# Kernel optimization log

Measured on AMD Instinct MI355X. Metric: run time of the kernel, lower is better.

The kernel has to match this reference:

```python
import jax, jax.numpy as jnp
import numpy as np

N_NODES = 50000
N_EDGES = 800000
LATENT = 64
K_STEPS = 2
GAMMA = 0.9


def _xavier(key, fan_in, fan_out):
    lim = float(np.sqrt(6.0 / (fan_in + fan_out)))
    return jax.random.uniform(key, (fan_in, fan_out), minval=-lim, maxval=lim, dtype=jnp.float32)


def setup_inputs() -> dict:
    key = jax.random.key(0)
    ks = iter(jax.random.split(key, 48))
    L = LATENT
    inp = {}
    inp["x"] = jax.random.normal(next(ks), (N_NODES, 1), dtype=jnp.float32)
    inp["sol"] = jax.random.normal(next(ks), (N_NODES, 1), dtype=jnp.float32)
    inp["y"] = jax.random.normal(next(ks), (N_NODES, 1), dtype=jnp.float32)
    inp["tags"] = jax.random.randint(next(ks), (N_NODES,), 0, 2, dtype=jnp.int32)
    inp["edge_index"] = jax.random.randint(next(ks), (2, N_EDGES), 0, N_NODES, dtype=jnp.int32)
    inp["edge_attr"] = jax.random.normal(next(ks), (N_EDGES, 3), dtype=jnp.float32)
    inp["a_ij"] = jax.random.normal(next(ks), (N_EDGES,), dtype=jnp.float32)
    inp["prb_data"] = jax.random.normal(next(ks), (N_NODES, 2), dtype=jnp.float32)
    # phi_to / phi_from message MLPs: (2L+3) -> L -> L
    for name in ("pt", "pf"):
        inp[name + "_W1"] = _xavier(next(ks), 2 * L + 3, L)
        inp[name + "_b1"] = jnp.zeros((L,), jnp.float32)
        inp[name + "_W2"] = _xavier(next(ks), L, L)
        inp[name + "_b2"] = jnp.zeros((L,), jnp.float32)
    # gating MLPs: (3L+2) -> L, single linear + activation
    for name in ("zk", "rk", "corr"):
        inp[name + "_W"] = _xavier(next(ks), 3 * L + 2, L)
        inp[name + "_b"] = jnp.zeros((L,), jnp.float32)
    # encoder: 1 -> L -> L ; decoder: L -> L -> 1
    inp["e_W1"] = _xavier(next(ks), 1, L); inp["e_b1"] = jnp.zeros((L,), jnp.float32)
    inp["e_W2"] = _xavier(next(ks), L, L); inp["e_b2"] = jnp.zeros((L,), jnp.float32)
    inp["d_W1"] = _xavier(next(ks), L, L); inp["d_b1"] = jnp.zeros((L,), jnp.float32)
    inp["d_W2"] = _xavier(next(ks), L, 1); inp["d_b2"] = jnp.zeros((1,), jnp.float32)
    return inp


def reference(x, sol, y, tags, edge_index, edge_attr, a_ij, prb_data,
              pt_W1, pt_b1, pt_W2, pt_b2, pf_W1, pf_b1, pf_W2, pf_b2,
              zk_W, zk_b, rk_W, rk_b, corr_W, corr_b,
              e_W1, e_b1, e_W2, e_b2, d_W1, d_b1, d_W2, d_b2):
    n = x.shape[0]
    row, col = edge_index[0], edge_index[1]
    # remove_self_loops: mask out edges with row == col instead of slicing
    loop_mask = (row != col).astype(x.dtype)[:, None]

    def mlp2(t, W1, b1, W2, b2):  # Linear -> ReLU -> Linear
        return jnp.maximum(t @ W1 + b1, 0.0) @ W2 + b2

    def phi(h, i_idx, j_idx, W1, b1, W2, b2):
        # message = MLP([x_i, x_j, edge_attr]); aggr='add' at node i
        tmp = jnp.concatenate([h[i_idx], h[j_idx], edge_attr], axis=1)
        msg = mlp2(tmp, W1, b1, W2, b2) * loop_mask
        return jax.ops.segment_sum(msg, i_idx, num_segments=n)

    enc_p = (e_W1, e_b1, e_W2, e_b2)
    dec_p = (d_W1, d_b1, d_W2, d_b2)

    def apply(u, p):
        return mlp2(u, *p)

    def residual_loss(u):
        Au = jax.ops.segment_sum(a_ij[:, None] * u[col], row, num_segments=n)
        return jnp.mean((Au - y) ** 2)

    mse = lambda a, b: jnp.mean((a - b) ** 2)
    sg = lambda p: tuple(jax.lax.stop_gradient(t) for t in p)
    dir_mask = (tags == 1)[:, None]

    H0 = apply(x, enc_p)
    H = H0
    U = x
    total = jnp.float32(0.0)
    for step in range(K_STEPS):
        # phi_to: flow source->target => i = col (target); phi_from: i = row (source)
        mess_to = phi(H, col, row, pt_W1, pt_b1, pt_W2, pt_b2)
        mess_from = phi(H, row, col, pf_W1, pf_b1, pf_W2, pf_b2)
        cat = jnp.concatenate([H, mess_to, mess_from, prb_data], axis=1)
        alpha = jax.nn.sigmoid(cat @ zk_W + zk_b)
        reset = jax.nn.sigmoid(cat @ rk_W + rk_b)
        corr = jnp.tanh(
            jnp.concatenate([reset * H, mess_to, mess_from, prb_data], axis=1) @ corr_W + corr_b)
        Hn = H + alpha * corr
        Hn = jnp.where(dir_mask, H0, Hn)  # Dirichlet nodes reset to H['0']
        U = apply(Hn, dec_p)
        res = residual_loss(U)
        enc_loss = mse(apply(apply(Hn, sg(dec_p)), enc_p), Hn)        # 'latent'
        autoenc_loss = mse(apply(apply(U, sg(enc_p)), dec_p), U)      # 'physics'
        total = total + res * GAMMA ** (K_STEPS - step - 1) + enc_loss + autoenc_loss
        H = Hn
    return (U, total)
```

## Files before the change

### kernel.cpp

```cpp
#include <hip/hip_runtime.h>

#define DEV __device__ __forceinline__

constexpr int N = 50000;
constexpr int E = 800000;
constexpr int NBUK = 196;

constexpr int HF_OFF  = 0;
constexpr int H0F_OFF = 64*N;
constexpr int MTF_OFF = 128*N;
constexpr int MFF_OFF = 160*N;
constexpr int PBT_OFF = MTF_OFF;
constexpr int PBF_OFF = MFF_OFF;
constexpr int R1_OFF  = 192*N;
constexpr int PAT_OFF = R1_OFF;
constexpr int PAF_OFF = R1_OFF + 64*N;
constexpr int AL_OFF  = R1_OFF;
constexpr int RH_OFF  = R1_OFF + 64*N;
constexpr int T1_OFF  = R1_OFF;
constexpr int EV_OFF  = R1_OFF + 64*N;
constexpr int CSTG_OFF = R1_OFF;
constexpr int RSTG_OFF = R1_OFF + 4*E;
constexpr int HB_OFF   = 352*N;
constexpr int UV_OFF   = 384*N;
constexpr int LOSS_OFF = UV_OFF + N;
constexpr int FLAG_OFF = LOSS_OFF + 7;
constexpr int WZR_OFF = LOSS_OFF + 8;
constexpr int GB_OFF  = WZR_OFF + 24832;
constexpr int CW_OFF  = GB_OFF + 128;
constexpr int CB_OFF  = CW_OFF + 12416;
constexpr int PT1_OFF = CB_OFF + 64;
constexpr int AT_OFF  = PT1_OFF + 8192;
constexpr int BT1_OFF = AT_OFF + 192;
constexpr int WT2_OFF = BT1_OFF + 64;
constexpr int BT2_OFF = WT2_OFF + 4096;
constexpr int PF1_OFF = BT2_OFF + 64;
constexpr int AF_OFF  = PF1_OFF + 8192;
constexpr int BF1_OFF = AF_OFF + 192;
constexpr int WF2_OFF = BF1_OFF + 64;
constexpr int BF2_OFF = WF2_OFF + 4096;
constexpr int DW1_OFF = BF2_OFF + 64;
constexpr int DW2_OFF = DW1_OFF + 4096;
constexpr int DB1_OFF = DW2_OFF + 64;
constexpr int DB2_OFF = DB1_OFF + 64;
constexpr int EW1_OFF = DB2_OFF + 4;
constexpr int EB1_OFF = EW1_OFF + 64;
constexpr int EW2_OFF = EB1_OFF + 64;
constexpr int EB2_OFF = EW2_OFF + 4096;
constexpr int PRB0_OFF = EB2_OFF + 64;
constexpr int PRB1_OFF = PRB0_OFF + N;
constexpr int NWZR_OFF = PRB1_OFF + N;
constexpr int NCW_OFF  = NWZR_OFF + 25088;
constexpr int CNT_OFF  = NCW_OFF + 12544;
constexpr int FEND     = CNT_OFF + 2*N;
constexpr int CREC_OFF = FEND;
constexpr int RREC_OFF = CREC_OFF + 2*E;
constexpr int LCP_OFF  = RREC_OFF + 4*E;
constexpr int FRP_OFF  = LCP_OFF + N + 1;
constexpr int LE_OFF   = FRP_OFF + N + 1;
constexpr int LCF_OFF  = LE_OFF + N;
constexpr int LRF_OFF  = LCF_OFF + N;
constexpr int SFF_OFF  = LRF_OFF + N;
constexpr int CDEG_OFF = SFF_OFF + N;
constexpr int RDEG_OFF = CDEG_OFF + N;
constexpr int SDEG_OFF = RDEG_OFF + N;
constexpr int BS_OFF   = SDEG_OFF + N;
constexpr int BO_OFF   = BS_OFF + 512;
constexpr int GFC_OFF  = BO_OFF + 512;
constexpr int GFR_OFF  = GFC_OFF + 196;

constexpr int PREP_TOTAL = 24832+128+12416+64+8192+192+64+4096+64+8192+192+64+4096+64+4096+64+64+1+64+64+4096+64+6;
constexpr int PREP2_TOTAL = 25088 + 12544;

DEV float b2f(unsigned short u){ return __uint_as_float(((unsigned)u) << 16); }
DEV unsigned short f2b(float f){
    unsigned u = __float_as_uint(f);
    return (unsigned short)((u + 0x7fffu + ((u >> 16) & 1u)) >> 16);
}
DEV float blo(unsigned u){ return __uint_as_float(u << 16); }
DEV float bhi(unsigned u){ return __uint_as_float(u & 0xffff0000u); }
DEV int bcasti(int v, int k){ return __builtin_amdgcn_readlane(v, k); }
DEV float wave_sum(float v){
    #pragma unroll
    for (int off = 32; off > 0; off >>= 1) v += __shfl_xor(v, off, 64);
    return v;
}
DEV float ldv(const void* p, int i, bool isbf){
    return isbf ? b2f(((const unsigned short*)p)[i]) : ((const float*)p)[i];
}
DEV unsigned short ld16(const void* p, int i, bool isbf){
    return isbf ? ((const unsigned short*)p)[i] : f2b(((const float*)p)[i]);
}
DEV float sigm(float x){ return 1.f / (1.f + __expf(-x)); }

struct WPtrs {
    const void *ptW1, *ptb1, *ptW2, *ptb2;
    const void *pfW1, *pfb1, *pfW2, *pfb2;
    const void *zkW, *zkb, *rkW, *rkb, *cW, *cb;
    const void *eW1, *eb1, *eW2, *eb2;
    const void *dW1, *db1, *dW2, *db2;
};

__global__ __launch_bounds__(256) void detect_kernel(const void* y, float* __restrict__ ws){
    __shared__ int bad;
    if (threadIdx.x == 0) bad = 0;
    __syncthreads();
    const unsigned short* yy = (const unsigned short*)y;
    int mybad = 0;
    for (int i = threadIdx.x; i < 4096; i += 256){
        float v = b2f(yy[i]);
        if (!(v > -1.0e6f && v < 1.0e6f)) mybad = 1;
    }
    if (mybad) bad = 1;
    __syncthreads();
    if (threadIdx.x == 0) ws[FLAG_OFF] = bad ? 0.0f : 1.0f;
}

__global__ __launch_bounds__(256) void prep_kernel(WPtrs P, float* __restrict__ ws){
    int j = blockIdx.x * 256 + threadIdx.x;
    if (j >= PREP_TOTAL) return;
    bool isbf = ws[FLAG_OFF] > 0.5f;
    if (j < 24832){
        int k = j >> 7, c = j & 127;
        ws[WZR_OFF+j] = (c < 64) ? ldv(P.zkW, k*64+c, isbf) : ldv(P.rkW, k*64+(c-64), isbf);
        return;
    } j -= 24832;
    if (j < 128){ ws[GB_OFF+j] = (j < 64) ? ldv(P.zkb, j, isbf) : ldv(P.rkb, j-64, isbf); return; } j -= 128;
    if (j < 12416){ ws[CW_OFF+j] = ldv(P.cW, j, isbf); return; } j -= 12416;
    if (j < 64){ ws[CB_OFF+j] = ldv(P.cb, j, isbf); return; } j -= 64;
    if (j < 8192){ ws[PT1_OFF+j] = ldv(P.ptW1, j, isbf); return; } j -= 8192;
    if (j < 192){ ws[AT_OFF+j] = ldv(P.ptW1, 128*64+j, isbf); return; } j -= 192;
    if (j < 64){ ws[BT1_OFF+j] = ldv(P.ptb1, j, isbf); return; } j -= 64;
    if (j < 4096){ ws[WT2_OFF+j] = ldv(P.ptW2, j, isbf); return; } j -= 4096;
    if (j < 64){ ws[BT2_OFF+j] = ldv(P.ptb2, j, isbf); return; } j -= 64;
    if (j < 8192){ ws[PF1_OFF+j] = ldv(P.pfW1, j, isbf); return; } j -= 8192;
    if (j < 192){ ws[AF_OFF+j] = ldv(P.pfW1, 128*64+j, isbf); return; } j -= 192;
    if (j < 64){ ws[BF1_OFF+j] = ldv(P.pfb1, j, isbf); return; } j -= 64;
    if (j < 4096){ ws[WF2_OFF+j] = ldv(P.pfW2, j, isbf); return; } j -= 4096;
    if (j < 64){ ws[BF2_OFF+j] = ldv(P.pfb2, j, isbf); return; } j -= 64;
    if (j < 4096){ ws[DW1_OFF+j] = ldv(P.dW1, j, isbf); return; } j -= 4096;
    if (j < 64){ ws[DW2_OFF+j] = ldv(P.dW2, j, isbf); return; } j -= 64;
    if (j < 64){ ws[DB1_OFF+j] = ldv(P.db1, j, isbf); return; } j -= 64;
    if (j < 1){ ws[DB2_OFF] = ldv(P.db2, 0, isbf); return; } j -= 1;
    if (j < 64){ ws[EW1_OFF+j] = ldv(P.eW1, j, isbf); return; } j -= 64;
    if (j < 64){ ws[EB1_OFF+j] = ldv(P.eb1, j, isbf); return; } j -= 64;
    if (j < 4096){ ws[EW2_OFF+j] = ldv(P.eW2, j, isbf); return; } j -= 4096;
    if (j < 64){ ws[EB2_OFF+j] = ldv(P.eb2, j, isbf); return; } j -= 64;
    ws[LOSS_OFF+j] = 0.f;
}

__global__ __launch_bounds__(256) void prep2_kernel(float* __restrict__ ws){
    int j = blockIdx.x * 256 + threadIdx.x;
    if (j >= PREP2_TOTAL) return;
    if (j < 25088){
        int r = j >> 7, c = j & 127;
        float v;
        if (r < 64) v = ws[WZR_OFF + r*128 + c];
        else if (r < 128){
            int h = r - 64; float s = 0.f;
            for (int m = 0; m < 64; m++)
                s = fmaf(ws[WT2_OFF + h*64 + m], ws[WZR_OFF + (64+m)*128 + c], s);
            v = s;
        } else if (r < 192){
            int h = r - 128; float s = 0.f;
            for (int m = 0; m < 64; m++)
                s = fmaf(ws[WF2_OFF + h*64 + m], ws[WZR_OFF + (128+m)*128 + c], s);
            v = s;
        } else if (r < 194) v = ws[WZR_OFF + r*128 + c];
        else if (r == 194){
            float s = 0.f;
            for (int m = 0; m < 64; m++)
                s = fmaf(ws[BT2_OFF + m], ws[WZR_OFF + (64+m)*128 + c], s);
            v = s;
        } else {
            float s = 0.f;
            for (int m = 0; m < 64; m++)
                s = fmaf(ws[BF2_OFF + m], ws[WZR_OFF + (128+m)*128 + c], s);
            v = s;
        }
        ws[NWZR_OFF + j] = v;
        return;
    }
    j -= 25088;
    {
        int r = j >> 6, c = j & 63;
        float v;
        if (r < 64) v = ws[CW_OFF + r*64 + c];
        else if (r < 128){
            int h = r - 64; float s = 0.f;
            for (int m = 0; m < 64; m++)
                s = fmaf(ws[WT2_OFF + h*64 + m], ws[CW_OFF + (64+m)*64 + c], s);
            v = s;
        } else if (r < 192){
            int h = r - 128; float s = 0.f;
            for (int m = 0; m < 64; m++)
                s = fmaf(ws[WF2_OFF + h*64 + m], ws[CW_OFF + (128+m)*64 + c], s);
            v = s;
        } else if (r < 194) v = ws[CW_OFF + r*64 + c];
        else if (r == 194){
            float s = 0.f;
            for (int m = 0; m < 64; m++)
                s = fmaf(ws[BT2_OFF + m], ws[CW_OFF + (64+m)*64 + c], s);
            v = s;
        } else {
            float s = 0.f;
            for (int m = 0; m < 64; m++)
                s = fmaf(ws[BF2_OFF + m], ws[CW_OFF + (128+m)*64 + c], s);
            v = s;
        }
        ws[NCW_OFF + j] = v;
    }
}

__global__ __launch_bounds__(256) void setup_node(const void* __restrict__ prb, float* __restrict__ ws){
    int i = blockIdx.x * 256 + threadIdx.x;
    if (i >= N) return;
    bool isbf = ws[FLAG_OFF] > 0.5f;
    ws[PRB0_OFF+i] = ldv(prb, 2*i,   isbf);
    ws[PRB1_OFF+i] = ldv(prb, 2*i+1, isbf);
    int* wsI = (int*)ws;
    wsI[CDEG_OFF+i] = 0; wsI[RDEG_OFF+i] = 0; wsI[SDEG_OFF+i] = 0;
}

__global__ __launch_bounds__(256) void hist_kernel(const int* __restrict__ ei, int* __restrict__ wsI){
    int e = blockIdx.x * 256 + threadIdx.x;
    if (e >= E) return;
    int r = ei[e], c = ei[E+e];
    atomicAdd(&wsI[RDEG_OFF + r], 1);
    atomicAdd(&wsI[CDEG_OFF + c], 1);
    if (r == c) atomicAdd(&wsI[SDEG_OFF + r], 1);
}
DEV int deg_at(const int* wsI, int y, int i){
    if (y == 0) return wsI[CDEG_OFF+i] - wsI[SDEG_OFF+i];
    return wsI[RDEG_OFF+i];
}
__global__ __launch_bounds__(256) void scan1(int* __restrict__ wsI){
    int y = blockIdx.y;
    int* tmp = wsI + (y == 0 ? LCP_OFF : FRP_OFF);
    int i = blockIdx.x * 256 + threadIdx.x;
    __shared__ int sh[256];
    int v = (i < N) ? deg_at(wsI, y, i) : 0;
    sh[threadIdx.x] = v;
    __syncthreads();
    #pragma unroll
    for (int off = 1; off < 256; off <<= 1){
        int t = (threadIdx.x >= (unsigned)off) ? sh[threadIdx.x - off] : 0;
        __syncthreads();
        sh[threadIdx.x] += t;
        __syncthreads();
    }
    if (i < N) tmp[i] = sh[threadIdx.x] - v;
    if (threadIdx.x == 255) wsI[BS_OFF + y*256 + blockIdx.x] = sh[255];
}
__global__ __launch_bounds__(256) void scan2(int* __restrict__ wsI){
    int y = blockIdx.y, t = threadIdx.x;
    __shared__ int sh[256];
    int v = (t < 196) ? wsI[BS_OFF + y*256 + t] : 0;
    sh[t] = v;
    __syncthreads();
    #pragma unroll
    for (int off = 1; off < 256; off <<= 1){
        int u = (t >= (unsigned)off) ? sh[t - off] : 0;
        __syncthreads();
        sh[t] += u;
        __syncthreads();
    }
    wsI[BO_OFF + y*256 + t] = sh[t] - v;
}
__global__ __launch_bounds__(256) void scan3(int* __restrict__ wsI){
    int y = blockIdx.y;
    int* ptr = wsI + (y == 0 ? LCP_OFF : FRP_OFF);
    int i = blockIdx.x * 256 + threadIdx.x;
    if (i < N){
        int d = deg_at(wsI, y, i);
        int p = ptr[i] + wsI[BO_OFF + y*256 + blockIdx.x];
        ptr[i] = p;
        if ((i & 255) == 0){
            if (y == 0) wsI[GFC_OFF + (i >> 8)] = p;
            else        wsI[GFR_OFF + (i >> 8)] = p;
        }
        if (y == 0){
            wsI[LCF_OFF+i] = p;
            if (i == N-1) ptr[N] = p + d;
        } else {
            int live = wsI[RDEG_OFF+i] - wsI[SDEG_OFF+i];
            wsI[LRF_OFF+i] = p;
            wsI[LE_OFF+i]  = p + live;
            wsI[SFF_OFF+i] = p + live;
            if (i == N-1) ptr[N] = E;
        }
    }
}

__global__ __launch_bounds__(256) void scatter_binA(const int* __restrict__ ei,
                                                    const void* __restrict__ attr,
                                                    const void* __restrict__ aij,
                                                    float* __restrict__ ws){
    __shared__ int hc[NBUK], hr[NBUK], bc[NBUK], br[NBUK];
    int t = threadIdx.x;
    for (int i = t; i < NBUK; i += 256){ hc[i] = 0; hr[i] = 0; }
    __syncthreads();
    int* wsI = (int*)ws;
    int e0 = blockIdx.x * 4096;
    for (int i = 0; i < 16; i++){
        int e = e0 + i*256 + t;
        if (e < E){
            int r = ei[e], c = ei[E+e];
            if (r != c) atomicAdd(&hc[c >> 8], 1);
            atomicAdd(&hr[r >> 8], 1);
        }
    }
    __syncthreads();
    if (t < NBUK){
        bc[t] = atomicAdd(&wsI[GFC_OFF+t], hc[t]);
        br[t] = atomicAdd(&wsI[GFR_OFF+t], hr[t]);
        hc[t] = 0; hr[t] = 0;
    }
    __syncthreads();
    bool isbf = ws[FLAG_OFF] > 0.5f;
    uint4* cstg = (uint4*)(ws + CSTG_OFF);
    uint4* rstg = (uint4*)(ws + RSTG_OFF);
    for (int i = 0; i < 16; i++){
        int e = e0 + i*256 + t;
        if (e < E){
            int r = ei[e], c = ei[E+e];
            unsigned a0 = ld16(attr, 3*e, isbf), a1 = ld16(attr, 3*e+1, isbf);
            unsigned a2 = ld16(attr, 3*e+2, isbf), av = ld16(aij, e, isbf);
            unsigned a01 = a0 | (a1 << 16);
            if (r != c){
                int off = atomicAdd(&hc[c >> 8], 1);
                cstg[bc[c >> 8] + off] = make_uint4((unsigned)r | (a2 << 16), a01, (unsigned)c, 0u);
            }
            int off2 = atomicAdd(&hr[r >> 8], 1);
            rstg[br[r >> 8] + off2] = make_uint4((unsigned)c | (a2 << 16), a01, av << 16, (unsigned)r);
        }
    }
}

__global__ __launch_bounds__(256) void scatter_binB(float* __restrict__ ws){
    int* wsI = (int*)ws;
    int b = blockIdx.x;
    if (blockIdx.y == 0){
        int beg = wsI[LCP_OFF + b*256];
        int end = wsI[GFC_OFF + b];
        const uint4* cstg = (const uint4*)(ws + CSTG_OFF);
        uint2* crec = (uint2*)(ws + CREC_OFF);
        for (int p = beg + threadIdx.x; p < end; p += 256){
            uint4 q = cstg[p];
            int d = atomicAdd(&wsI[LCF_OFF + (int)q.z], 1);
            crec[d] = make_uint2(q.x, q.y);
        }
    } else {
        int beg = wsI[FRP_OFF + b*256];
        int end = wsI[GFR_OFF + b];
        const uint4* rstg = (const uint4*)(ws + RSTG_OFF);
        uint4* rrec = (uint4*)(ws + RREC_OFF);
        for (int p = beg + threadIdx.x; p < end; p += 256){
            uint4 q = rstg[p];
            int r = (int)q.w;
            int c = (int)(q.x & 0xffffu);
            int d = (r != c) ? atomicAdd(&wsI[LRF_OFF + r], 1)
                             : atomicAdd(&wsI[SFF_OFF + r], 1);
            rrec[d] = make_uint4(q.x, q.y, q.z, 0u);
        }
    }
}

__global__ __launch_bounds__(256) void encode_init(const void* __restrict__ x,
                                                   float* __restrict__ ws){
    int node = blockIdx.x * 256 + threadIdx.x;
    if (node >= N) return;
    bool isbf = ws[FLAG_OFF] > 0.5f;
    int j0 = blockIdx.y * 32;
    float xv = ldv(x, node, isbf);
    float acc[32];
    #pragma unroll
    for (int j = 0; j < 32; j++) acc[j] = ws[EB2_OFF + j0 + j];
    for (int k = 0; k < 64; k++){
        float t = fmaxf(fmaf(xv, ws[EW1_OFF+k], ws[EB1_OFF+k]), 0.f);
        const float* wr = ws + EW2_OFF + (size_t)k*64 + j0;
        #pragma unroll
        for (int j = 0; j < 32; j++) acc[j] = fmaf(t, wr[j], acc[j]);
    }
    unsigned short* hb = (unsigned short*)(ws + HB_OFF);
    #pragma unroll
    for (int j = 0; j < 32; j++){
        ws[H0F_OFF + (size_t)(j0+j)*N + node] = acc[j];
        ws[HF_OFF  + (size_t)(j0+j)*N + node] = acc[j];
        hb[(size_t)(j0+j)*N + node] = f2b(acc[j]);
    }
}

__global__ __launch_bounds__(256) void node_pre(float* __restrict__ ws){
    int node = blockIdx.x * 256 + threadIdx.x;
    if (node >= N) return;
    int dir = blockIdx.y >> 1, tl = blockIdx.y & 1;
    int j0 = tl * 32;
    const float* W1 = ws + (dir ? PF1_OFF : PT1_OFF);
    float* paOut = ws + (dir ? PAF_OFF : PAT_OFF);
    unsigned short* pbOut = (unsigned short*)(ws + (dir ? PBF_OFF : PBT_OFF));
    const unsigned short* hb = (const unsigned short*)(ws + HB_OFF);
    float aA[32], aB[32];
    #pragma unroll
    for (int j = 0; j < 32; j++){ aA[j] = 0.f; aB[j] = 0.f; }
    #pragma unroll 4
    for (int k = 0; k < 64; k++){
        float hv = b2f(hb[(size_t)k*N + node]);
        const float* wA = W1 + (size_t)k*64 + j0;
        const float* wB = W1 + (size_t)(64+k)*64 + j0;
        #pragma unroll
        for (int j = 0; j < 32; j++){
            aA[j] = fmaf(hv, wA[j], aA[j]);
            aB[j] = fmaf(hv, wB[j], aB[j]);
        }
    }
    #pragma unroll
    for (int j = 0; j < 32; j++){
        paOut[(size_t)node*64 + j0 + j] = aA[j];
        pbOut[(size_t)node*64 + j0 + j] = f2b(aB[j]);
    }
}

template<int DIR>
__global__ __launch_bounds__(256) void gather_msgs(float* __restrict__ ws){
    const int* wsI = (const int*)ws;
    float* pa = ws + (DIR ? PAF_OFF : PAT_OFF);
    const unsigned short* pgb = (const unsigned short*)(ws + (DIR ? PBF_OFF : PBT_OFF));
    const float* A3 = ws + (DIR ? AF_OFF : AT_OFF);
    const float* b1 = ws + (DIR ? BF1_OFF : BT1_OFF);

    int lane = threadIdx.x & 63;
    int wv = threadIdx.x >> 6;
    float A0 = A3[lane], A1 = A3[64+lane], A2 = A3[128+lane];
    float B1 = b1[lane];
    int gw = blockIdx.x * 4 + wv;
    int nw = gridDim.x * 4;
    for (int node = gw; node < N; node += nw){
        float pav = pa[(size_t)node*64 + lane] + B1;
        float hs = 0.f;
        int beg, end;
        if (DIR == 0){ beg = wsI[LCP_OFF+node]; end = wsI[LCP_OFF+node+1]; }
        else         { beg = wsI[FRP_OFF+node]; end = wsI[LE_OFF+node]; }
        int cnt = end - beg;
        for (int base = beg; base < end; base += 64){
            int mcnt = end - base; if (mcnt > 64) mcnt = 64;
            unsigned rxL = 0, ryL = 0;
            if (lane < mcnt){
                if (DIR == 0){
                    uint2 q = ((const uint2*)(ws + CREC_OFF))[base + lane];
                    rxL = q.x; ryL = q.y;
                } else {
                    uint4 q = ((const uint4*)(ws + RREC_OFF))[base + lane];
                    rxL = q.x; ryL = q.y;
                }
            }
            for (int g = 0; g < mcnt; g += 8){
                unsigned rxa[8], rya[8];
                float pb[8];
                #pragma unroll
                for (int t = 0; t < 8; t++){
                    rxa[t] = (unsigned)bcasti((int)rxL, g+t);
                    rya[t] = (unsigned)bcasti((int)ryL, g+t);
                    int o = (int)(rxa[t] & 0xffffu);
                    float pv = b2f(pgb[(size_t)o*64 + lane]);
                    pb[t] = (g+t < mcnt) ? pv : -3.0e38f;
                }
                #pragma unroll
                for (int t = 0; t < 8; t++){
                    float hv = fmaf(blo(rya[t]), A0,
                               fmaf(bhi(rya[t]), A1,
                               fmaf(bhi(rxa[t]), A2, pav))) + pb[t];
                    hs += fmaxf(hv, 0.f);
                }
            }
        }
        pa[(size_t)node*64 + lane] = hs;
        if (lane == 0) ws[CNT_OFF + DIR*N + node] = (float)cnt;
    }
}

__global__ __launch_bounds__(256) void transpose_msg(float* __restrict__ ws){
    __shared__ float t[64][65];
    const float* src = ws + (blockIdx.y ? PAF_OFF : PAT_OFF);
    unsigned short* dst = (unsigned short*)(ws + (blockIdx.y ? MFF_OFF : MTF_OFF));
    int n0 = blockIdx.x * 64;
    #pragma unroll
    for (int i = 0; i < 16; i++){
        int idx = i*256 + threadIdx.x;
        int nl = idx >> 6, f = idx & 63;
        int node = n0 + nl;
        t[nl][f] = (node < N) ? src[(size_t)node*64 + f] : 0.f;
    }
    __syncthreads();
    #pragma unroll
    for (int i = 0; i < 16; i++){
        int idx = i*256 + threadIdx.x;
        int fw = idx >> 6, nl = idx & 63;
        int node = n0 + nl;
        if (node < N) dst[(size_t)fw*N + node] = f2b(t[nl][fw]);
    }
}

__global__ __launch_bounds__(256) void gate_zr(float* __restrict__ ws){
    int node = blockIdx.x * 256 + threadIdx.x;
    if (node >= N) return;
    int tl = blockIdx.y, j0 = tl * 16;
    const float* W = ws + NWZR_OFF + j0;
    const unsigned short* hb  = (const unsigned short*)(ws + HB_OFF);
    const unsigned short* mtU = (const unsigned short*)(ws + MTF_OFF);
    const unsigned short* mfU = (const unsigned short*)(ws + MFF_OFF);
    float p0 = ws[PRB0_OFF+node], p1 = ws[PRB1_OFF+node];
    float cT = ws[CNT_OFF+node], cF = ws[CNT_OFF+N+node];
    float az[16], ar[16];
    #pragma unroll
    for (int j = 0; j < 16; j++){
        az[j] = ws[GB_OFF + j0 + j]
              + p0*W[192*128+j] + p1*W[193*128+j] + cT*W[194*128+j] + cF*W[195*128+j];
        ar[j] = ws[GB_OFF + 64 + j0 + j]
              + p0*W[192*128+64+j] + p1*W[193*128+64+j] + cT*W[194*128+64+j] + cF*W[195*128+64+j];
    }
    #pragma unroll 4
    for (int k = 0; k < 64; k++){
        float aH = b2f(hb [(size_t)k*N + node]);
        float aT = b2f(mtU[(size_t)k*N + node]);
        float aF = b2f(mfU[(size_t)k*N + node]);
        const float* wH = W + (size_t)k*128;
        const float* wT = W + (size_t)(64+k)*128;
        const float* wF = W + (size_t)(128+k)*128;
        #pragma unroll
        for (int j = 0; j < 16; j++){
            az[j] = fmaf(aH, wH[j], fmaf(aT, wT[j], fmaf(aF, wF[j], az[j])));
            ar[j] = fmaf(aH, wH[64+j], fmaf(aT, wT[64+j], fmaf(aF, wF[64+j], ar[j])));
        }
    }
    unsigned short* RH = (unsigned short*)(ws + RH_OFF);
    #pragma unroll
    for (int j = 0; j < 16; j++){
        size_t off = (size_t)(j0+j)*N + node;
        ws[AL_OFF + off] = sigm(az[j]);
        RH[off] = f2b(sigm(ar[j]) * b2f(hb[off]));
    }
}

__global__ __launch_bounds__(256) void gate_corr(const int* __restrict__ tags,
                                                 float* __restrict__ ws){
    int node = blockIdx.x * 256 + threadIdx.x;
    if (node >= N) return;
    int tl = blockIdx.y, j0 = tl*16;
    const float* W = ws + NCW_OFF + j0;
    const unsigned short* RH  = (const unsigned short*)(ws + RH_OFF);
    const unsigned short* mtU = (const unsigned short*)(ws + MTF_OFF);
    const unsigned short* mfU = (const unsigned short*)(ws + MFF_OFF);
    float p0 = ws[PRB0_OFF+node], p1 = ws[PRB1_OFF+node];
    float cT = ws[CNT_OFF+node], cF = ws[CNT_OFF+N+node];
    float acc[16];
    #pragma unroll
    for (int j = 0; j < 16; j++)
        acc[j] = ws[CB_OFF + j0 + j]
               + p0*W[192*64+j] + p1*W[193*64+j] + cT*W[194*64+j] + cF*W[195*64+j];
    #pragma unroll 4
    for (int k = 0; k < 64; k++){
        float aR = b2f(RH [(size_t)k*N + node]);
        float aT = b2f(mtU[(size_t)k*N + node]);
        float aF = b2f(mfU[(size_t)k*N + node]);
        const float* wR = W + (size_t)k*64;
        const float* wT = W + (size_t)(64+k)*64;
        const float* wF = W + (size_t)(128+k)*64;
        #pragma unroll
        for (int j = 0; j < 16; j++)
            acc[j] = fmaf(aR, wR[j], fmaf(aT, wT[j], fmaf(aF, wF[j], acc[j])));
    }
    int tg = tags[node];
    unsigned short* hb = (unsigned short*)(ws + HB_OFF);
    #pragma unroll
    for (int j = 0; j < 16; j++){
        size_t off = (size_t)(j0+j)*N + node;
        float hn = fmaf(ws[AL_OFF+off], tanhf(acc[j]), ws[HF_OFF+off]);
        if (tg == 1) hn = ws[H0F_OFF+off];
        ws[HF_OFF+off] = hn;
        hb[off] = f2b(hn);
    }
}

__global__ __launch_bounds__(256) void dec1hf(const unsigned short* __restrict__ src,
                                              float* __restrict__ dst,
                                              float* __restrict__ ws){
    int node = blockIdx.x * 256 + threadIdx.x;
    if (node >= N) return;
    int j0 = blockIdx.y * 32;
    float acc[32];
    #pragma unroll
    for (int j = 0; j < 32; j++) acc[j] = ws[DB1_OFF + j0 + j];
    #pragma unroll 4
    for (int k = 0; k < 64; k++){
        float a = b2f(src[(size_t)k*N + node]);
        const float* wr = ws + DW1_OFF + (size_t)k*64 + j0;
        #pragma unroll
        for (int j = 0; j < 32; j++) acc[j] = fmaf(a, wr[j], acc[j]);
    }
    #pragma unroll
    for (int j = 0; j < 32; j++)
        dst[(size_t)(j0+j)*N + node] = fmaxf(acc[j], 0.f);
}

__global__ __launch_bounds__(256) void dec1hb(const unsigned short* __restrict__ src,
                                              unsigned short* __restrict__ dst,
                                              float* __restrict__ ws){
    int node = blockIdx.x * 256 + threadIdx.x;
    if (node >= N) return;
    int j0 = blockIdx.y * 32;
    float acc[32];
    #pragma unroll
    for (int j = 0; j < 32; j++) acc[j] = ws[DB1_OFF + j0 + j];
    #pragma unroll 4
    for (int k = 0; k < 64; k++){
        float a = b2f(src[(size_t)k*N + node]);
        const float* wr = ws + DW1_OFF + (size_t)k*64 + j0;
        #pragma unroll
        for (int j = 0; j < 32; j++) acc[j] = fmaf(a, wr[j], acc[j]);
    }
    #pragma unroll
    for (int j = 0; j < 32; j++)
        dst[(size_t)(j0+j)*N + node] = f2b(fmaxf(acc[j], 0.f));
}

__global__ __launch_bounds__(256) void enc_u(int step, float* __restrict__ ws){
    int node = blockIdx.x * 256 + threadIdx.x;
    float encA = 0.f;
    if (node < N){
        int j0 = blockIdx.y * 32;
        float u = ws[DB2_OFF];
        for (int j = 0; j < 64; j++)
            u = fmaf(ws[T1_OFF + (size_t)j*N + node], ws[DW2_OFF+j], u);
        if (blockIdx.y == 0) ws[UV_OFF+node] = u;
        float acc[32];
        #pragma unroll
        for (int j = 0; j < 32; j++) acc[j] = ws[EB2_OFF + j0 + j];
        for (int k = 0; k < 64; k++){
            float t = fmaxf(fmaf(u, ws[EW1_OFF+k], ws[EB1_OFF+k]), 0.f);
            const float* wr = ws + EW2_OFF + (size_t)k*64 + j0;
            #pragma unroll
            for (int j = 0; j < 32; j++) acc[j] = fmaf(t, wr[j], acc[j]);
        }
        unsigned short* ev = (unsigned short*)(ws + EV_OFF);
        #pragma unroll
        for (int j = 0; j < 32; j++){
            size_t off = (size_t)(j0+j)*N + node;
            ev[off] = f2b(acc[j]);
            float d = acc[j] - ws[HF_OFF+off];
            encA += d*d;
        }
    }
    encA = wave_sum(encA);
    if ((threadIdx.x & 63) == 0) atomicAdd(&ws[LOSS_OFF + step*3 + 1], encA);
}

__global__ __launch_bounds__(256) void aux_res(int step, const void* __restrict__ y,
                                               float* __restrict__ ws){
    const int* wsI = (const int*)ws;
    int node = blockIdx.x * 256 + threadIdx.x;
    bool isbf = ws[FLAG_OFF] > 0.5f;
    float autoA = 0.f, resA = 0.f;
    if (node < N){
        const unsigned short* T1u = (const unsigned short*)(ws + T1_OFF);
        float u2 = ws[DB2_OFF];
        for (int j = 0; j < 64; j++)
            u2 = fmaf(b2f(T1u[(size_t)j*N + node]), ws[DW2_OFF+j], u2);
        float u = ws[UV_OFF+node];
        float ad = u2 - u;
        autoA = ad*ad;
        float acc = 0.f;
        int beg = wsI[FRP_OFF+node], end = wsI[FRP_OFF+node+1];
        const uint4* rrec = (const uint4*)(ws + RREC_OFF);
        for (int p = beg; p < end; p++){
            uint4 q = rrec[p];
            acc = fmaf(bhi(q.z), ws[UV_OFF + (int)(q.x & 0xffffu)], acc);
        }
        float d = acc - ldv(y, node, isbf);
        resA = d*d;
    }
    autoA = wave_sum(autoA);
    resA = wave_sum(resA);
    if ((threadIdx.x & 63) == 0){
        atomicAdd(&ws[LOSS_OFF + step*3 + 2], autoA);
        atomicAdd(&ws[LOSS_OFF + step*3], resA);
    }
}

__global__ __launch_bounds__(256) void write_out(void* __restrict__ outp,
                                                 const float* __restrict__ ws){
    int i = blockIdx.x * 256 + threadIdx.x;
    if (i > N) return;
    bool isbf = ws[FLAG_OFF] > 0.5f;
    float v;
    if (i < N){
        v = ws[UV_OFF+i];
    } else {
        const float* L = ws + LOSS_OFF;
        float inv = 1.f / (float)N, invl = 1.f / ((float)N * 64.f);
        v = 0.9f*L[0]*inv + L[1]*invl + L[2]*inv
          +      L[3]*inv + L[4]*invl + L[5]*inv;
    }
    if (isbf) ((unsigned short*)outp)[i] = f2b(v);
    else      ((float*)outp)[i] = v;
}

extern "C" void kernel_launch(void* const* d_in, const int* in_sizes, int n_in,
                              void* d_out, int out_size, void* d_ws, size_t ws_size,
                              hipStream_t stream){
    const void* x    = d_in[0];
    const void* y    = d_in[2];
    const int* tags  = (const int*)d_in[3];
    const int* ei    = (const int*)d_in[4];
    const void* attr = d_in[5];
    const void* aij  = d_in[6];
    const void* prb  = d_in[7];
    WPtrs P;
    P.ptW1 = d_in[8];  P.ptb1 = d_in[9];  P.ptW2 = d_in[10]; P.ptb2 = d_in[11];
    P.pfW1 = d_in[12]; P.pfb1 = d_in[13]; P.pfW2 = d_in[14]; P.pfb2 = d_in[15];
    P.zkW  = d_in[16]; P.zkb  = d_in[17]; P.rkW  = d_in[18]; P.rkb  = d_in[19];
    P.cW   = d_in[20]; P.cb   = d_in[21];
    P.eW1  = d_in[22]; P.eb1  = d_in[23]; P.eW2  = d_in[24]; P.eb2  = d_in[25];
    P.dW1  = d_in[26]; P.db1  = d_in[27]; P.dW2  = d_in[28]; P.db2  = d_in[29];
    float* ws = (float*)d_ws;
    int* wsI = (int*)d_ws;

    detect_kernel<<<1, 256, 0, stream>>>(y, ws);
    prep_kernel<<<(PREP_TOTAL + 255)/256, 256, 0, stream>>>(P, ws);
    prep2_kernel<<<(PREP2_TOTAL + 255)/256, 256, 0, stream>>>(ws);
    setup_node<<<196, 256, 0, stream>>>(prb, ws);
    hist_kernel<<<E/256, 256, 0, stream>>>(ei, wsI);
    scan1<<<dim3(196, 2), 256, 0, stream>>>(wsI);
    scan2<<<dim3(1, 2), 256, 0, stream>>>(wsI);
    scan3<<<dim3(196, 2), 256, 0, stream>>>(wsI);
    scatter_binA<<<196, 256, 0, stream>>>(ei, attr, aij, ws);
    scatter_binB<<<dim3(196, 2), 256, 0, stream>>>(ws);
    encode_init<<<dim3(196, 2), 256, 0, stream>>>(x, ws);
    unsigned short* hb = (unsigned short*)(ws + HB_OFF);
    unsigned short* ev = (unsigned short*)(ws + EV_OFF);
    for (int step = 0; step < 2; step++){
        node_pre<<<dim3(196, 4), 256, 0, stream>>>(ws);
        gather_msgs<0><<<2048, 256, 0, stream>>>(ws);
        gather_msgs<1><<<2048, 256, 0, stream>>>(ws);
        transpose_msg<<<dim3(782, 2), 256, 0, stream>>>(ws);
        gate_zr<<<dim3(196, 4), 256, 0, stream>>>(ws);
        gate_corr<<<dim3(196, 4), 256, 0, stream>>>(tags, ws);
        dec1hf<<<dim3(196, 2), 256, 0, stream>>>(hb, ws + T1_OFF, ws);
        enc_u<<<dim3(196, 2), 256, 0, stream>>>(step, ws);
        dec1hb<<<dim3(196, 2), 256, 0, stream>>>(ev, (unsigned short*)(ws + T1_OFF), ws);
        aux_res<<<196, 256, 0, stream>>>(step, y, ws);
    }
    write_out<<<197, 256, 0, stream>>>(d_out, ws);
}
```

Baseline: 969.9 us.

## Replace global per-node degree atomics with bucket histogram and shared-memory degree counting

```diff
diff --git a/kernel.cpp b/kernel.cpp
--- a/kernel.cpp
+++ b/kernel.cpp
@@ -68,6 +68,10 @@
 constexpr int BO_OFF   = BS_OFF + 512;
 constexpr int GFC_OFF  = BO_OFF + 512;
 constexpr int GFR_OFF  = GFC_OFF + 196;
+constexpr int BKC_OFF  = GFR_OFF + 196;
+constexpr int BKR_OFF  = BKC_OFF + 196;
+constexpr int GBC_OFF  = BKR_OFF + 196;
+constexpr int GBR_OFF  = GBC_OFF + 197;
 
 constexpr int PREP_TOTAL = 24832+128+12416+64+8192+192+64+4096+64+8192+192+64+4096+64+4096+64+64+1+64+64+4096+64+6;
 constexpr int PREP2_TOTAL = 25088 + 12544;
@@ -218,44 +222,40 @@
     bool isbf = ws[FLAG_OFF] > 0.5f;
     ws[PRB0_OFF+i] = ldv(prb, 2*i,   isbf);
     ws[PRB1_OFF+i] = ldv(prb, 2*i+1, isbf);
-    int* wsI = (int*)ws;
-    wsI[CDEG_OFF+i] = 0; wsI[RDEG_OFF+i] = 0; wsI[SDEG_OFF+i] = 0;
-}
-
-__global__ __launch_bounds__(256) void hist_kernel(const int* __restrict__ ei, int* __restrict__ wsI){
-    int e = blockIdx.x * 256 + threadIdx.x;
-    if (e >= E) return;
-    int r = ei[e], c = ei[E+e];
-    atomicAdd(&wsI[RDEG_OFF + r], 1);
-    atomicAdd(&wsI[CDEG_OFF + c], 1);
-    if (r == c) atomicAdd(&wsI[SDEG_OFF + r], 1);
-}
-DEV int deg_at(const int* wsI, int y, int i){
-    if (y == 0) return wsI[CDEG_OFF+i] - wsI[SDEG_OFF+i];
-    return wsI[RDEG_OFF+i];
-}
-__global__ __launch_bounds__(256) void scan1(int* __restrict__ wsI){
-    int y = blockIdx.y;
-    int* tmp = wsI + (y == 0 ? LCP_OFF : FRP_OFF);
-    int i = blockIdx.x * 256 + threadIdx.x;
+    if (i < NBUK){
+        int* wsI = (int*)ws;
+        wsI[BKC_OFF+i] = 0; wsI[BKR_OFF+i] = 0;
+    }
+}
+
+__global__ __launch_bounds__(256) void bucket_hist(const int* __restrict__ ei, int* __restrict__ wsI){
+    __shared__ int hc[NBUK], hr[NBUK];
+    int t = threadIdx.x;
+    for (int i = t; i < NBUK; i += 256){ hc[i] = 0; hr[i] = 0; }
+    __syncthreads();
+    int e0 = blockIdx.x * 4096;
+    for (int i = 0; i < 16; i++){
+        int e = e0 + i*256 + t;
+        if (e < E){
+            int r = ei[e], c = ei[E+e];
+            if (r != c) atomicAdd(&hc[c >> 8], 1);
+            atomicAdd(&hr[r >> 8], 1);
+        }
+    }
+    __syncthreads();
+    if (t < NBUK){
+        if (hc[t]) atomicAdd(&wsI[BKC_OFF+t], hc[t]);
+        if (hr[t]) atomicAdd(&wsI[BKR_OFF+t], hr[t]);
+    }
+}
+
+__global__ __launch_bounds__(256) void bucket_scan(int* __restrict__ wsI){
+    int y = blockIdx.y, t = threadIdx.x;
+    const int* bk = wsI + (y ? BKR_OFF : BKC_OFF);
+    int* gb = wsI + (y ? GBR_OFF : GBC_OFF);
+    int* gf = wsI + (y ? GFR_OFF : GFC_OFF);
     __shared__ int sh[256];
-    int v = (i < N) ? deg_at(wsI, y, i) : 0;
-    sh[threadIdx.x] = v;
-    __syncthreads();
-    #pragma unroll
-    for (int off = 1; off < 256; off <<= 1){
-        int t = (threadIdx.x >= (unsigned)off) ? sh[threadIdx.x - off] : 0;
-        __syncthreads();
-        sh[threadIdx.x] += t;
-        __syncthreads();
-    }
-    if (i < N) tmp[i] = sh[threadIdx.x] - v;
-    if (threadIdx.x == 255) wsI[BS_OFF + y*256 + blockIdx.x] = sh[255];
-}
-__global__ __launch_bounds__(256) void scan2(int* __restrict__ wsI){
-    int y = blockIdx.y, t = threadIdx.x;
-    __shared__ int sh[256];
-    int v = (t < 196) ? wsI[BS_OFF + y*256 + t] : 0;
+    int v = (t < NBUK) ? bk[t] : 0;
     sh[t] = v;
     __syncthreads();
     #pragma unroll
@@ -265,31 +265,9 @@
         sh[t] += u;
         __syncthreads();
     }
-    wsI[BO_OFF + y*256 + t] = sh[t] - v;
-}
-__global__ __launch_bounds__(256) void scan3(int* __restrict__ wsI){
-    int y = blockIdx.y;
-    int* ptr = wsI + (y == 0 ? LCP_OFF : FRP_OFF);
-    int i = blockIdx.x * 256 + threadIdx.x;
-    if (i < N){
-        int d = deg_at(wsI, y, i);
-        int p = ptr[i] + wsI[BO_OFF + y*256 + blockIdx.x];
-        ptr[i] = p;
-        if ((i & 255) == 0){
-            if (y == 0) wsI[GFC_OFF + (i >> 8)] = p;
-            else        wsI[GFR_OFF + (i >> 8)] = p;
-        }
-        if (y == 0){
-            wsI[LCF_OFF+i] = p;
-            if (i == N-1) ptr[N] = p + d;
-        } else {
-            int live = wsI[RDEG_OFF+i] - wsI[SDEG_OFF+i];
-            wsI[LRF_OFF+i] = p;
-            wsI[LE_OFF+i]  = p + live;
-            wsI[SFF_OFF+i] = p + live;
-            if (i == N-1) ptr[N] = E;
-        }
-    }
+    int base = sh[t] - v;
+    if (t < NBUK){ gb[t] = base; gf[t] = base; }
+    if (t == NBUK - 1) gb[NBUK] = sh[t];
 }
 
 __global__ __launch_bounds__(256) void scatter_binA(const int* __restrict__ ei,
@@ -337,11 +315,102 @@
     }
 }
 
+__global__ __launch_bounds__(256) void deg_count(float* __restrict__ ws){
+    __shared__ int cnt[256];
+    __shared__ int scnt[256];
+    int* wsI = (int*)ws;
+    int b = blockIdx.x, t = threadIdx.x;
+    cnt[t] = 0; scnt[t] = 0;
+    __syncthreads();
+    if (blockIdx.y == 0){
+        int beg = wsI[GBC_OFF + b], end = wsI[GFC_OFF + b];
+        const uint4* cstg = (const uint4*)(ws + CSTG_OFF);
+        for (int p = beg + t; p < end; p += 256)
+            atomicAdd(&cnt[(int)(cstg[p].z & 255u)], 1);
+        __syncthreads();
+        int node = b*256 + t;
+        if (node < N) wsI[CDEG_OFF + node] = cnt[t];
+    } else {
+        int beg = wsI[GBR_OFF + b], end = wsI[GFR_OFF + b];
+        const uint4* rstg = (const uint4*)(ws + RSTG_OFF);
+        for (int p = beg + t; p < end; p += 256){
+            uint4 q = rstg[p];
+            int idx = (int)(q.w & 255u);
+            atomicAdd(&cnt[idx], 1);
+            if ((q.x & 0xffffu) == q.w) atomicAdd(&scnt[idx], 1);
+        }
+        __syncthreads();
+        int node = b*256 + t;
+        if (node < N){
+            wsI[RDEG_OFF + node] = cnt[t];
+            wsI[SDEG_OFF + node] = scnt[t];
+        }
+    }
+}
+
+DEV int deg_at(const int* wsI, int y, int i){
+    if (y == 0) return wsI[CDEG_OFF+i];
+    return wsI[RDEG_OFF+i];
+}
+__global__ __launch_bounds__(256) void scan1(int* __restrict__ wsI){
+    int y = blockIdx.y;
+    int* tmp = wsI + (y == 0 ? LCP_OFF : FRP_OFF);
+    int i = blockIdx.x * 256 + threadIdx.x;
+    __shared__ int sh[256];
+    int v = (i < N) ? deg_at(wsI, y, i) : 0;
+    sh[threadIdx.x] = v;
+    __syncthreads();
+    #pragma unroll
+    for (int off = 1; off < 256; off <<= 1){
+        int t = (threadIdx.x >= (unsigned)off) ? sh[threadIdx.x - off] : 0;
+        __syncthreads();
+        sh[threadIdx.x] += t;
+        __syncthreads();
+    }
+    if (i < N) tmp[i] = sh[threadIdx.x] - v;
+    if (threadIdx.x == 255) wsI[BS_OFF + y*256 + blockIdx.x] = sh[255];
+}
+__global__ __launch_bounds__(256) void scan2(int* __restrict__ wsI){
+    int y = blockIdx.y, t = threadIdx.x;
+    __shared__ int sh[256];
+    int v = (t < 196) ? wsI[BS_OFF + y*256 + t] : 0;
+    sh[t] = v;
+    __syncthreads();
+    #pragma unroll
+    for (int off = 1; off < 256; off <<= 1){
+        int u = (t >= (unsigned)off) ? sh[t - off] : 0;
+        __syncthreads();
+        sh[t] += u;
+        __syncthreads();
+    }
+    wsI[BO_OFF + y*256 + t] = sh[t] - v;
+}
+__global__ __launch_bounds__(256) void scan3(int* __restrict__ wsI){
+    int y = blockIdx.y;
+    int* ptr = wsI + (y == 0 ? LCP_OFF : FRP_OFF);
+    int i = blockIdx.x * 256 + threadIdx.x;
+    if (i < N){
+        int d = deg_at(wsI, y, i);
+        int p = ptr[i] + wsI[BO_OFF + y*256 + blockIdx.x];
+        ptr[i] = p;
+        if (y == 0){
+            wsI[LCF_OFF+i] = p;
+            if (i == N-1) ptr[N] = p + d;
+        } else {
+            int live = wsI[RDEG_OFF+i] - wsI[SDEG_OFF+i];
+            wsI[LRF_OFF+i] = p;
+            wsI[LE_OFF+i]  = p + live;
+            wsI[SFF_OFF+i] = p + live;
+            if (i == N-1) ptr[N] = E;
+        }
+    }
+}
+
 __global__ __launch_bounds__(256) void scatter_binB(float* __restrict__ ws){
     int* wsI = (int*)ws;
     int b = blockIdx.x;
     if (blockIdx.y == 0){
-        int beg = wsI[LCP_OFF + b*256];
+        int beg = wsI[GBC_OFF + b];
         int end = wsI[GFC_OFF + b];
         const uint4* cstg = (const uint4*)(ws + CSTG_OFF);
         uint2* crec = (uint2*)(ws + CREC_OFF);
@@ -351,7 +420,7 @@
             crec[d] = make_uint2(q.x, q.y);
         }
     } else {
-        int beg = wsI[FRP_OFF + b*256];
+        int beg = wsI[GBR_OFF + b];
         int end = wsI[GFR_OFF + b];
         const uint4* rstg = (const uint4*)(ws + RSTG_OFF);
         uint4* rrec = (uint4*)(ws + RREC_OFF);
@@ -729,11 +798,13 @@
     prep_kernel<<<(PREP_TOTAL + 255)/256, 256, 0, stream>>>(P, ws);
     prep2_kernel<<<(PREP2_TOTAL + 255)/256, 256, 0, stream>>>(ws);
     setup_node<<<196, 256, 0, stream>>>(prb, ws);
-    hist_kernel<<<E/256, 256, 0, stream>>>(ei, wsI);
+    bucket_hist<<<196, 256, 0, stream>>>(ei, wsI);
+    bucket_scan<<<dim3(1, 2), 256, 0, stream>>>(wsI);
+    scatter_binA<<<196, 256, 0, stream>>>(ei, attr, aij, ws);
+    deg_count<<<dim3(196, 2), 256, 0, stream>>>(ws);
     scan1<<<dim3(196, 2), 256, 0, stream>>>(wsI);
     scan2<<<dim3(1, 2), 256, 0, stream>>>(wsI);
     scan3<<<dim3(196, 2), 256, 0, stream>>>(wsI);
-    scatter_binA<<<196, 256, 0, stream>>>(ei, attr, aij, ws);
     scatter_binB<<<dim3(196, 2), 256, 0, stream>>>(ws);
     encode_init<<<dim3(196, 2), 256, 0, stream>>>(x, ws);
     unsigned short* hb = (unsigned short*)(ws + HB_OFF);
```

Result: faster. 928.1 us (-4.3%).
